# Kernel optimization log

Measured on AMD Instinct MI355X. Metric: run time of the kernel, lower is better.

The kernel has to match this reference:

```python
import jax, jax.numpy as jnp
import numpy as np

B, S, HIDDEN = 2, 2048, 1024
NUM_HEADS, HEAD_DIM = 16, 64
STRIDE = 128
NEG = -10000.0


def _strided_mask(seq_len):
    # Sparse Transformer strided pattern: causal, local window of STRIDE,
    # plus every STRIDE-th previous position.
    i = jnp.arange(seq_len)[:, None]
    j = jnp.arange(seq_len)[None, :]
    diff = i - j
    allowed = (diff >= 0) & ((diff < STRIDE) | (diff % STRIDE == 0))
    return jnp.where(allowed, 0.0, NEG).astype(jnp.float32)  # [S, S]


def setup_inputs() -> dict:
    key = jax.random.key(0)
    k0, k1, k2, k3, k4 = jax.random.split(key, 5)
    hidden_states = jax.random.normal(k0, (B, S, HIDDEN), dtype=jnp.float32)
    attention_mask = jnp.zeros((B, 1, 1, S), dtype=jnp.float32)
    W_q = jax.random.normal(k1, (HIDDEN, HIDDEN), dtype=jnp.float32) * 0.02
    b_q = jnp.zeros((HIDDEN,), dtype=jnp.float32)
    W_v = jax.random.normal(k2, (HIDDEN, HIDDEN), dtype=jnp.float32) * 0.02
    b_v = jnp.zeros((HIDDEN,), dtype=jnp.float32)
    return {"hidden_states": hidden_states, "attention_mask": attention_mask,
            "W_q": W_q, "b_q": b_q, "W_v": W_v, "b_v": b_v}


def _heads(x):
    b, s, _ = x.shape
    return x.reshape(b, s, NUM_HEADS, HEAD_DIM).transpose(0, 2, 1, 3)  # [B,H,S,d]


def reference(hidden_states, attention_mask, W_q, b_q, W_v, b_v):
    q = _heads(hidden_states @ W_q + b_q)  # [B,H,S,d]
    v = _heads(hidden_states @ W_v + b_v)  # [B,H,S,d]
    hash_mask = _strided_mask(q.shape[-2])  # [S,S], broadcast over B,H
    # NB: source computes matmul(query, query^T) -- Q used for both sides.
    scores = jnp.einsum('bhid,bhjd->bhij', q, q) + hash_mask
    scores = scores / jnp.sqrt(jnp.asarray(HEAD_DIM, scores.dtype))
    scores = scores + attention_mask
    probs = jax.nn.softmax(scores, axis=-1)  # dropout p=0 (eval)
    ctx = jnp.einsum('bhij,bhjd->bhid', probs, v)  # [B,H,S,d]
    b = ctx.shape[0]
    return ctx.transpose(0, 2, 1, 3).reshape(b, -1, NUM_HEADS * HEAD_DIM)
```

## Files before the change

### kernel.cpp

```cpp
#include <hip/hip_runtime.h>

typedef __attribute__((ext_vector_type(8))) short short8;
typedef __attribute__((ext_vector_type(4))) float float4v;

__device__ inline float bf2f(ushort u) {
    unsigned v = ((unsigned)u) << 16;
    return __builtin_bit_cast(float, v);
}
__device__ inline ushort f2bf(float f) {
    unsigned u = __builtin_bit_cast(unsigned, f);
    u += 0x7FFFu + ((u >> 16) & 1u);
    return (ushort)(u >> 16);
}

__global__ __launch_bounds__(256) void transpose_w(
    const float* __restrict__ Wq, const float* __restrict__ Wv,
    ushort* __restrict__ Wtq, ushort* __restrict__ Wtv) {
    __shared__ ushort tile[64][68];
    const float* W = blockIdx.z ? Wv : Wq;
    ushort* Wt     = blockIdx.z ? Wtv : Wtq;
    const int k0 = blockIdx.y * 64, n0 = blockIdx.x * 64;
    const int tid = threadIdx.x;
    const int rr = tid >> 4;
    const int cc = (tid & 15) * 4;
    union U4 { ushort u[4]; uint2 v; };
#pragma unroll
    for (int i = 0; i < 4; ++i) {
        int row = rr + i * 16;
        float4v f = *(const float4v*)(W + (size_t)(k0 + row) * 1024 + n0 + cc);
        U4 x;
#pragma unroll
        for (int j = 0; j < 4; ++j) x.u[j] = f2bf(f[j]);
        *(uint2*)&tile[row][cc] = x.v;
    }
    __syncthreads();
#pragma unroll
    for (int i = 0; i < 4; ++i) {
        int row = rr + i * 16;
        U4 o;
#pragma unroll
        for (int j = 0; j < 4; ++j) o.u[j] = tile[cc + j][row];
        *(uint2*)(Wt + (size_t)(n0 + row) * 1024 + k0 + cc) = o.v;
    }
}

__global__ __launch_bounds__(256) void qv_gemm(
    const float* __restrict__ hs,
    const ushort* __restrict__ Wtq, const ushort* __restrict__ Wtv,
    const float* __restrict__ bq, const float* __restrict__ bv,
    ushort* __restrict__ q_ws, ushort* __restrict__ v_ws) {
    __shared__ ushort Al[128][72];
    __shared__ ushort Bl[128][72];
    const ushort* Wt  = blockIdx.z ? Wtv : Wtq;
    const float* bias = blockIdx.z ? bv : bq;
    ushort* out       = blockIdx.z ? v_ws : q_ws;
    const int m0 = blockIdx.y * 128;
    const int n0 = blockIdx.x * 128;
    const int tid = threadIdx.x;
    const int wid = tid >> 6, lane = tid & 63;
    const int quad = lane >> 4, l16 = lane & 15;
    const int wm = (wid >> 1) * 64, wn = (wid & 1) * 64;

    float4v acc[4][4] = {};

    for (int kt = 0; kt < 1024; kt += 64) {
        __syncthreads();
#pragma unroll
        for (int i = 0; i < 4; ++i) {
            int c = tid + i * 256;
            int row = c >> 3, col = (c & 7) * 8;
            const float* src = hs + (size_t)(m0 + row) * 1024 + kt + col;
            float4v f0 = *(const float4v*)(src);
            float4v f1 = *(const float4v*)(src + 4);
            union { ushort u[8]; uint4 v; } pk;
#pragma unroll
            for (int j = 0; j < 4; ++j) { pk.u[j] = f2bf(f0[j]); pk.u[4 + j] = f2bf(f1[j]); }
            *(uint4*)&Al[row][col] = pk.v;
            *(uint4*)&Bl[row][col] = *(const uint4*)(Wt + (size_t)(n0 + row) * 1024 + kt + col);
        }
        __syncthreads();
#pragma unroll
        for (int ks = 0; ks < 2; ++ks) {
            short8 af[4], bfr[4];
#pragma unroll
            for (int mt = 0; mt < 4; ++mt)
                af[mt] = *(const short8*)&Al[wm + mt * 16 + l16][ks * 32 + quad * 8];
#pragma unroll
            for (int nt = 0; nt < 4; ++nt)
                bfr[nt] = *(const short8*)&Bl[wn + nt * 16 + l16][ks * 32 + quad * 8];
#pragma unroll
            for (int mt = 0; mt < 4; ++mt)
#pragma unroll
                for (int nt = 0; nt < 4; ++nt)
                    acc[mt][nt] = __builtin_amdgcn_mfma_f32_16x16x32_bf16(
                        af[mt], bfr[nt], acc[mt][nt], 0, 0, 0);
        }
    }
#pragma unroll
    for (int mt = 0; mt < 4; ++mt) {
#pragma unroll
        for (int nt = 0; nt < 4; ++nt) {
            int coln = n0 + wn + nt * 16 + l16;
            float bsv = bias[coln];
            int hh = coln >> 6, dd = coln & 63;
#pragma unroll
            for (int reg = 0; reg < 4; ++reg) {
                int r = m0 + wm + mt * 16 + quad * 4 + reg;
                int bb = r >> 11, s = r & 2047;
                out[(((size_t)bb * 16 + hh) * 2048 + s) * 64 + dd] =
                    f2bf(acc[mt][nt][reg] + bsv);
            }
        }
    }
}

__global__ __launch_bounds__(512) void attn(
    const ushort* __restrict__ q_ws, const ushort* __restrict__ v_ws,
    const float* __restrict__ amask, float* __restrict__ out) {
    const int t = blockIdx.x, h = blockIdx.y, b = blockIdx.z;

    __shared__ ushort Kw[256][72];
    __shared__ ushort Vt[64][266];
    __shared__ ushort Pl[128][266];
    __shared__ float  Sstr[128][17];
    __shared__ float  am[2048];

    const int tid = threadIdx.x;
    const int wid = tid >> 6, lane = tid & 63;
    const int quad = lane >> 4, l16 = lane & 15;
    const int r0 = wid * 16;
    const size_t qbase = ((size_t)b * 16 + h) * 2048 * 64;
    const int base_row = (t - 1) * 128;
    const int nk = (t >= 2) ? (t - 1) : 0;

    *(float4v*)&am[tid * 4] = *(const float4v*)(amask + (size_t)b * 2048 + tid * 4);
#pragma unroll
    for (int i = 0; i < 4; ++i) {
        int c = tid + i * 512;
        int row = c >> 3, col = (c & 7) * 8;
        int jg = base_row + row; if (jg < 0) jg = 0;
        *(uint4*)&Kw[row][col] = *(const uint4*)(q_ws + qbase + (size_t)jg * 64 + col);
    }
    {
        int j = tid & 255, dh0 = (tid >> 8) * 32;
        int jg = base_row + j; if (jg < 0) jg = 0;
        const ushort* src = v_ws + qbase + (size_t)jg * 64 + dh0;
#pragma unroll
        for (int d = 0; d < 32; d += 8) {
            union { uint4 v; ushort u[8]; } tmp;
            tmp.v = *(const uint4*)(src + d);
#pragma unroll
            for (int jj = 0; jj < 8; ++jj) Vt[dh0 + d + jj][j] = tmp.u[jj];
        }
    }
    __syncthreads();

    float4v sacc[16] = {};
#pragma unroll
    for (int ks = 0; ks < 2; ++ks) {
        short8 af = *(const short8*)&Kw[128 + r0 + l16][ks * 32 + quad * 8];
#pragma unroll
        for (int nt = 0; nt < 16; ++nt) {
            short8 bfr = *(const short8*)&Kw[nt * 16 + l16][ks * 32 + quad * 8];
            sacc[nt] = __builtin_amdgcn_mfma_f32_16x16x32_bf16(af, bfr, sacc[nt], 0, 0, 0);
        }
    }

    const int sr = tid >> 2;
    const int dq = (tid & 3) * 16;
    if (nk > 0) {
        float qv[16];
#pragma unroll
        for (int d = 0; d < 16; d += 8) {
            union { uint4 v; ushort u[8]; } tmp;
            tmp.v = *(const uint4*)&Kw[128 + sr][dq + d];
#pragma unroll
            for (int j = 0; j < 8; ++j) qv[d + j] = bf2f(tmp.u[j]);
        }
        for (int k = 0; k < nk; ++k) {
            const ushort* kr = q_ws + qbase + (size_t)(k * 128 + sr) * 64 + dq;
            float p = 0.f;
#pragma unroll
            for (int d = 0; d < 16; d += 8) {
                union { uint4 v; ushort u[8]; } tmp;
                tmp.v = *(const uint4*)(kr + d);
#pragma unroll
                for (int jj = 0; jj < 8; ++jj) p += qv[d + jj] * bf2f(tmp.u[jj]);
            }
            p += __shfl_xor(p, 1);
            p += __shfl_xor(p, 2);
            if ((tid & 3) == 0)
                Sstr[sr][k] = p * 0.125f + am[k * 128 + sr];
        }
    }
    __syncthreads();

#pragma unroll
    for (int reg = 0; reg < 4; ++reg) {
        int rr = r0 + quad * 4 + reg;
        float sv[16];
#pragma unroll
        for (int nt = 0; nt < 16; ++nt) {
            int c = nt * 16 + l16;
            bool allowed = (c >= rr) && (c <= rr + 128) && (t > 0 || c >= 128);
            int ci = base_row + c; if (ci < 0) ci = 0;
            sv[nt] = allowed ? sacc[nt][reg] * 0.125f + am[ci] : -INFINITY;
        }
        float sstr_v = (l16 < nk) ? Sstr[rr][l16] : -INFINITY;
        float m = sstr_v;
#pragma unroll
        for (int nt = 0; nt < 16; ++nt) m = fmaxf(m, sv[nt]);
#pragma unroll
        for (int off = 1; off < 16; off <<= 1) m = fmaxf(m, __shfl_xor(m, off));

        float es = (l16 < nk) ? __expf(sstr_v - m) : 0.f;
        float sum = es;
#pragma unroll
        for (int nt = 0; nt < 16; ++nt) {
            float e = (sv[nt] == -INFINITY) ? 0.f : __expf(sv[nt] - m);
            sv[nt] = e; sum += e;
        }
#pragma unroll
        for (int off = 1; off < 16; off <<= 1) sum += __shfl_xor(sum, off);
        float rden = 1.f / sum;
#pragma unroll
        for (int nt = 0; nt < 16; ++nt)
            Pl[rr][nt * 16 + l16] = f2bf(sv[nt] * rden);
        if (l16 < nk)
            Sstr[rr][l16] = es * rden;
    }
    __syncthreads();

    float4v cacc[4] = {};
#pragma unroll
    for (int ks = 0; ks < 8; ++ks) {
        short8 af = *(const short8*)&Pl[r0 + l16][ks * 32 + quad * 8];
#pragma unroll
        for (int nt = 0; nt < 4; ++nt) {
            short8 bfr = *(const short8*)&Vt[nt * 16 + l16][ks * 32 + quad * 8];
            cacc[nt] = __builtin_amdgcn_mfma_f32_16x16x32_bf16(af, bfr, cacc[nt], 0, 0, 0);
        }
    }
    __syncthreads();

    float* ctxp = (float*)&Pl[0][0];
    {
        float acc16[16] = {};
        for (int k = 0; k < nk; ++k) {
            float p = Sstr[sr][k];
            const ushort* vr = v_ws + qbase + (size_t)(k * 128 + sr) * 64 + dq;
#pragma unroll
            for (int d = 0; d < 16; d += 8) {
                union { uint4 v; ushort u[8]; } tmp;
                tmp.v = *(const uint4*)(vr + d);
#pragma unroll
                for (int j = 0; j < 8; ++j) acc16[d + j] += p * bf2f(tmp.u[j]);
            }
        }
#pragma unroll
        for (int d = 0; d < 16; d += 4)
            *(float4v*)&ctxp[sr * 68 + dq + d] = *(const float4v*)&acc16[d];
    }
    __syncthreads();

    const size_t obase = ((size_t)b * 2048 + (size_t)t * 128) * 1024 + (size_t)h * 64;
#pragma unroll
    for (int nt = 0; nt < 4; ++nt)
#pragma unroll
        for (int reg = 0; reg < 4; ++reg) {
            int rr = r0 + quad * 4 + reg;
            int d = nt * 16 + l16;
            out[obase + (size_t)rr * 1024 + d] = cacc[nt][reg] + ctxp[rr * 68 + d];
        }
}

extern "C" void kernel_launch(void* const* d_in, const int* in_sizes, int n_in,
                              void* d_out, int out_size, void* d_ws, size_t ws_size,
                              hipStream_t stream) {
    int ihs = -1, iam = -1, iw1 = -1, iw2 = -1, ib1 = -1, ib2 = -1;
    for (int i = 0; i < n_in; ++i) {
        int s = in_sizes[i];
        if      (s == 4194304) { if (ihs < 0) ihs = i; }
        else if (s == 4096)    { if (iam < 0) iam = i; }
        else if (s == 1048576) { if (iw1 < 0) iw1 = i; else if (iw2 < 0) iw2 = i; }
        else if (s == 1024)    { if (ib1 < 0) ib1 = i; else if (ib2 < 0) ib2 = i; }
    }
    if (ihs < 0) ihs = 0; if (iam < 0) iam = 1;
    if (iw1 < 0) iw1 = 2; if (ib1 < 0) ib1 = 3;
    if (iw2 < 0) iw2 = 4; if (ib2 < 0) ib2 = 5;

    const float* hs    = (const float*)d_in[ihs];
    const float* amask = (const float*)d_in[iam];
    const float* Wq    = (const float*)d_in[iw1];
    const float* bq    = (const float*)d_in[ib1];
    const float* Wv    = (const float*)d_in[iw2];
    const float* bv    = (const float*)d_in[ib2];
    float* out = (float*)d_out;

    char* ws = (char*)d_ws;
    ushort* Wtq  = (ushort*)(ws);
    ushort* Wtv  = (ushort*)(ws + (1u << 21));
    ushort* q_ws = (ushort*)(ws + (2u << 21));
    ushort* v_ws = (ushort*)(ws + (2u << 21) + (1u << 23));

    transpose_w<<<dim3(16, 16, 2), 256, 0, stream>>>(Wq, Wv, Wtq, Wtv);
    qv_gemm<<<dim3(8, 32, 2), 256, 0, stream>>>(hs, Wtq, Wtv, bq, bv, q_ws, v_ws);
    attn<<<dim3(16, 16, 2), 512, 0, stream>>>(q_ws, v_ws, amask, out);
}
```

Before: 157.5 us.

## Pre-convert hidden states, swizzle LDS tiles, and halve attention query tile

Adds a separate kernel that converts hidden states to bf16 once, so the GEMM no longer reconverts the same A tile for every N block and loads bf16 directly. The GEMM and attention shared-memory tiles switch from padded layouts to an XOR-swizzled layout to avoid bank conflicts. The attention kernel moves to 64-query tiles with 256 threads and a 192-key local window, which doubles the grid and trims wasted window work. Strided keys are now indexed per row modulo 128. The cost is one extra kernel launch and an extra global round trip for the converted activations.

```diff
diff --git a/kernel.cpp b/kernel.cpp
--- a/kernel.cpp
+++ b/kernel.cpp
@@ -11,6 +11,20 @@
     unsigned u = __builtin_bit_cast(unsigned, f);
     u += 0x7FFFu + ((u >> 16) & 1u);
     return (ushort)(u >> 16);
+}
+
+__global__ __launch_bounds__(256) void convert_hs(
+    const float* __restrict__ hs, ushort* __restrict__ hsb) {
+    const size_t base = ((size_t)blockIdx.x * 256 + threadIdx.x) * 16;
+    union { ushort u[16]; uint4 v[2]; } o;
+#pragma unroll
+    for (int q = 0; q < 4; ++q) {
+        float4v f = *(const float4v*)(hs + base + q * 4);
+#pragma unroll
+        for (int j = 0; j < 4; ++j) o.u[q * 4 + j] = f2bf(f[j]);
+    }
+    *(uint4*)(hsb + base)     = o.v[0];
+    *(uint4*)(hsb + base + 8) = o.v[1];
 }
 
 __global__ __launch_bounds__(256) void transpose_w(
@@ -45,17 +59,16 @@
 }
 
 __global__ __launch_bounds__(256) void qv_gemm(
-    const float* __restrict__ hs,
+    const ushort* __restrict__ hsb,
     const ushort* __restrict__ Wtq, const ushort* __restrict__ Wtv,
     const float* __restrict__ bq, const float* __restrict__ bv,
     ushort* __restrict__ q_ws, ushort* __restrict__ v_ws) {
-    __shared__ ushort Al[128][72];
-    __shared__ ushort Bl[128][72];
+    __shared__ ushort Al[128 * 64];
+    __shared__ ushort Bl[128 * 64];
     const ushort* Wt  = blockIdx.z ? Wtv : Wtq;
     const float* bias = blockIdx.z ? bv : bq;
     ushort* out       = blockIdx.z ? v_ws : q_ws;
-    const int m0 = blockIdx.y * 128;
-    const int n0 = blockIdx.x * 128;
+    const int m0 = blockIdx.y * 128, n0 = blockIdx.x * 128;
     const int tid = threadIdx.x;
     const int wid = tid >> 6, lane = tid & 63;
     const int quad = lane >> 4, l16 = lane & 15;
@@ -67,27 +80,28 @@
         __syncthreads();
 #pragma unroll
         for (int i = 0; i < 4; ++i) {
-            int c = tid + i * 256;
-            int row = c >> 3, col = (c & 7) * 8;
-            const float* src = hs + (size_t)(m0 + row) * 1024 + kt + col;
-            float4v f0 = *(const float4v*)(src);
-            float4v f1 = *(const float4v*)(src + 4);
-            union { ushort u[8]; uint4 v; } pk;
-#pragma unroll
-            for (int j = 0; j < 4; ++j) { pk.u[j] = f2bf(f0[j]); pk.u[4 + j] = f2bf(f1[j]); }
-            *(uint4*)&Al[row][col] = pk.v;
-            *(uint4*)&Bl[row][col] = *(const uint4*)(Wt + (size_t)(n0 + row) * 1024 + kt + col);
+            int u = tid + i * 256;
+            int row = u >> 3, c = u & 7;
+            int p = c ^ (row & 7);
+            *(uint4*)&Al[row * 64 + p * 8] =
+                *(const uint4*)(hsb + (size_t)(m0 + row) * 1024 + kt + c * 8);
+            *(uint4*)&Bl[row * 64 + p * 8] =
+                *(const uint4*)(Wt + (size_t)(n0 + row) * 1024 + kt + c * 8);
         }
         __syncthreads();
 #pragma unroll
         for (int ks = 0; ks < 2; ++ks) {
             short8 af[4], bfr[4];
 #pragma unroll
-            for (int mt = 0; mt < 4; ++mt)
-                af[mt] = *(const short8*)&Al[wm + mt * 16 + l16][ks * 32 + quad * 8];
-#pragma unroll
-            for (int nt = 0; nt < 4; ++nt)
-                bfr[nt] = *(const short8*)&Bl[wn + nt * 16 + l16][ks * 32 + quad * 8];
+            for (int mt = 0; mt < 4; ++mt) {
+                int row = wm + mt * 16 + l16;
+                af[mt] = *(const short8*)&Al[row * 64 + (((ks * 4 + quad) ^ (l16 & 7)) * 8)];
+            }
+#pragma unroll
+            for (int nt = 0; nt < 4; ++nt) {
+                int row = wn + nt * 16 + l16;
+                bfr[nt] = *(const short8*)&Bl[row * 64 + (((ks * 4 + quad) ^ (l16 & 7)) * 8)];
+            }
 #pragma unroll
             for (int mt = 0; mt < 4; ++mt)
 #pragma unroll
@@ -114,83 +128,105 @@
     }
 }
 
-__global__ __launch_bounds__(512) void attn(
+__global__ __launch_bounds__(256) void attn(
     const ushort* __restrict__ q_ws, const ushort* __restrict__ v_ws,
     const float* __restrict__ amask, float* __restrict__ out) {
+    __shared__ __align__(16) char smem[62464];
+    ushort (*Kw)[64]  = (ushort(*)[64])smem;
+    ushort (*Pl)[192] = (ushort(*)[192])smem;
+    float*  ctxp      = (float*)smem;
+    ushort (*Vt)[192] = (ushort(*)[192])(smem + 32768);
+    float  (*Sstr)[17] = (float(*)[17])(smem + 57344);
+    float*  amw       = (float*)(smem + 61696);
+
     const int t = blockIdx.x, h = blockIdx.y, b = blockIdx.z;
-
-    __shared__ ushort Kw[256][72];
-    __shared__ ushort Vt[64][266];
-    __shared__ ushort Pl[128][266];
-    __shared__ float  Sstr[128][17];
-    __shared__ float  am[2048];
-
     const int tid = threadIdx.x;
     const int wid = tid >> 6, lane = tid & 63;
     const int quad = lane >> 4, l16 = lane & 15;
     const int r0 = wid * 16;
     const size_t qbase = ((size_t)b * 16 + h) * 2048 * 64;
-    const int base_row = (t - 1) * 128;
-    const int nk = (t >= 2) ? (t - 1) : 0;
-
-    *(float4v*)&am[tid * 4] = *(const float4v*)(amask + (size_t)b * 2048 + tid * 4);
-#pragma unroll
-    for (int i = 0; i < 4; ++i) {
-        int c = tid + i * 512;
-        int row = c >> 3, col = (c & 7) * 8;
-        int jg = base_row + row; if (jg < 0) jg = 0;
-        *(uint4*)&Kw[row][col] = *(const uint4*)(q_ws + qbase + (size_t)jg * 64 + col);
-    }
-    {
-        int j = tid & 255, dh0 = (tid >> 8) * 32;
-        int jg = base_row + j; if (jg < 0) jg = 0;
-        const ushort* src = v_ws + qbase + (size_t)jg * 64 + dh0;
-#pragma unroll
-        for (int d = 0; d < 32; d += 8) {
-            union { uint4 v; ushort u[8]; } tmp;
-            tmp.v = *(const uint4*)(src + d);
-#pragma unroll
-            for (int jj = 0; jj < 8; ++jj) Vt[dh0 + d + jj][j] = tmp.u[jj];
-        }
-    }
-    __syncthreads();
-
-    float4v sacc[16] = {};
+    const int t0 = t * 64;
+    const int bc = t0 - 128;
+    const int cmin = (t == 0) ? 128 : (t == 1 ? 64 : 0);
+    const int nk = (t >= 4) ? ((t >> 1) - 1) : 0;
+
+    if (tid < 192) {
+        int j = bc + tid; if (j < 0) j = 0;
+        amw[tid] = amask[(size_t)b * 2048 + j];
+    }
+#pragma unroll
+    for (int i = 0; i < 8; ++i) {
+        int u = tid + i * 256;
+        int row = u >> 3, c = u & 7;
+        int jg = (row < 192) ? (bc + row) : (t0 + row - 192);
+        if (jg < 0) jg = 0;
+        int p = c ^ (row & 7);
+        *(uint4*)&Kw[row][p * 8] = *(const uint4*)(q_ws + qbase + (size_t)jg * 64 + c * 8);
+    }
+#pragma unroll
+    for (int i = 0; i < 2; ++i) {
+        int u = tid + i * 256;
+        if (u < 384) {
+            int j0 = (u % 48) * 4, d0 = (u / 48) * 8;
+            ushort vreg[4][8];
+#pragma unroll
+            for (int jj = 0; jj < 4; ++jj) {
+                int jg = bc + j0 + jj; if (jg < 0) jg = 0;
+                *(uint4*)vreg[jj] = *(const uint4*)(v_ws + qbase + (size_t)jg * 64 + d0);
+            }
+#pragma unroll
+            for (int dd = 0; dd < 8; ++dd) {
+                int row = d0 + dd;
+                int p = (j0 >> 3) ^ (row & 7);
+                union { ushort u4[4]; uint2 v; } pk;
+                pk.u4[0] = vreg[0][dd]; pk.u4[1] = vreg[1][dd];
+                pk.u4[2] = vreg[2][dd]; pk.u4[3] = vreg[3][dd];
+                *(uint2*)&Vt[row][p * 8 + (j0 & 7)] = pk.v;
+            }
+        }
+    }
+    __syncthreads();
+
+    float4v sacc[12] = {};
 #pragma unroll
     for (int ks = 0; ks < 2; ++ks) {
-        short8 af = *(const short8*)&Kw[128 + r0 + l16][ks * 32 + quad * 8];
-#pragma unroll
-        for (int nt = 0; nt < 16; ++nt) {
-            short8 bfr = *(const short8*)&Kw[nt * 16 + l16][ks * 32 + quad * 8];
+        int sw = ((ks * 4 + quad) ^ (l16 & 7)) * 8;
+        short8 af = *(const short8*)&Kw[192 + r0 + l16][sw];
+#pragma unroll
+        for (int nt = 0; nt < 12; ++nt) {
+            short8 bfr = *(const short8*)&Kw[nt * 16 + l16][sw];
             sacc[nt] = __builtin_amdgcn_mfma_f32_16x16x32_bf16(af, bfr, sacc[nt], 0, 0, 0);
         }
     }
 
     const int sr = tid >> 2;
     const int dq = (tid & 3) * 16;
+    const int smod = (t0 + sr) & 127;
     if (nk > 0) {
         float qv[16];
 #pragma unroll
-        for (int d = 0; d < 16; d += 8) {
-            union { uint4 v; ushort u[8]; } tmp;
-            tmp.v = *(const uint4*)&Kw[128 + sr][dq + d];
-#pragma unroll
-            for (int j = 0; j < 8; ++j) qv[d + j] = bf2f(tmp.u[j]);
-        }
-        for (int k = 0; k < nk; ++k) {
-            const ushort* kr = q_ws + qbase + (size_t)(k * 128 + sr) * 64 + dq;
+        for (int cc = 0; cc < 2; ++cc) {
+            int c = (dq >> 3) + cc;
+            int p = c ^ (sr & 7);
+            union { uint4 v; ushort u[8]; } tm;
+            tm.v = *(const uint4*)&Kw[192 + sr][p * 8];
+#pragma unroll
+            for (int jj = 0; jj < 8; ++jj) qv[cc * 8 + jj] = bf2f(tm.u[jj]);
+        }
+        for (int m = 0; m < nk; ++m) {
+            const ushort* kr = q_ws + qbase + (size_t)(smod + (m << 7)) * 64 + dq;
             float p = 0.f;
 #pragma unroll
             for (int d = 0; d < 16; d += 8) {
-                union { uint4 v; ushort u[8]; } tmp;
-                tmp.v = *(const uint4*)(kr + d);
-#pragma unroll
-                for (int jj = 0; jj < 8; ++jj) p += qv[d + jj] * bf2f(tmp.u[jj]);
+                union { uint4 v; ushort u[8]; } tm;
+                tm.v = *(const uint4*)(kr + d);
+#pragma unroll
+                for (int jj = 0; jj < 8; ++jj) p += qv[d + jj] * bf2f(tm.u[jj]);
             }
             p += __shfl_xor(p, 1);
             p += __shfl_xor(p, 2);
             if ((tid & 3) == 0)
-                Sstr[sr][k] = p * 0.125f + am[k * 128 + sr];
+                Sstr[sr][m] = p * 0.125f + amask[(size_t)b * 2048 + smod + (m << 7)];
         }
     }
     __syncthreads();
@@ -198,25 +234,24 @@
 #pragma unroll
     for (int reg = 0; reg < 4; ++reg) {
         int rr = r0 + quad * 4 + reg;
-        float sv[16];
-#pragma unroll
-        for (int nt = 0; nt < 16; ++nt) {
+        float sv[12];
+#pragma unroll
+        for (int nt = 0; nt < 12; ++nt) {
             int c = nt * 16 + l16;
-            bool allowed = (c >= rr) && (c <= rr + 128) && (t > 0 || c >= 128);
-            int ci = base_row + c; if (ci < 0) ci = 0;
-            sv[nt] = allowed ? sacc[nt][reg] * 0.125f + am[ci] : -INFINITY;
+            bool allowed = (c >= rr) && (c <= rr + 128) && (c >= cmin);
+            sv[nt] = allowed ? sacc[nt][reg] * 0.125f + amw[c] : -INFINITY;
         }
         float sstr_v = (l16 < nk) ? Sstr[rr][l16] : -INFINITY;
         float m = sstr_v;
 #pragma unroll
-        for (int nt = 0; nt < 16; ++nt) m = fmaxf(m, sv[nt]);
+        for (int nt = 0; nt < 12; ++nt) m = fmaxf(m, sv[nt]);
 #pragma unroll
         for (int off = 1; off < 16; off <<= 1) m = fmaxf(m, __shfl_xor(m, off));
 
         float es = (l16 < nk) ? __expf(sstr_v - m) : 0.f;
         float sum = es;
 #pragma unroll
-        for (int nt = 0; nt < 16; ++nt) {
+        for (int nt = 0; nt < 12; ++nt) {
             float e = (sv[nt] == -INFINITY) ? 0.f : __expf(sv[nt] - m);
             sv[nt] = e; sum += e;
         }
@@ -224,37 +259,40 @@
         for (int off = 1; off < 16; off <<= 1) sum += __shfl_xor(sum, off);
         float rden = 1.f / sum;
 #pragma unroll
-        for (int nt = 0; nt < 16; ++nt)
-            Pl[rr][nt * 16 + l16] = f2bf(sv[nt] * rden);
-        if (l16 < nk)
-            Sstr[rr][l16] = es * rden;
+        for (int nt = 0; nt < 12; ++nt) {
+            int c = nt * 16 + l16;
+            int p = ((c >> 3) ^ (rr & 7));
+            Pl[rr][p * 8 + (c & 7)] = f2bf(sv[nt] * rden);
+        }
+        if (l16 < nk) Sstr[rr][l16] = es * rden;
     }
     __syncthreads();
 
     float4v cacc[4] = {};
 #pragma unroll
-    for (int ks = 0; ks < 8; ++ks) {
-        short8 af = *(const short8*)&Pl[r0 + l16][ks * 32 + quad * 8];
+    for (int ks = 0; ks < 6; ++ks) {
+        int chunk = ks * 4 + quad;
+        int sw = (chunk ^ (l16 & 7)) * 8;
+        short8 af = *(const short8*)&Pl[r0 + l16][sw];
 #pragma unroll
         for (int nt = 0; nt < 4; ++nt) {
-            short8 bfr = *(const short8*)&Vt[nt * 16 + l16][ks * 32 + quad * 8];
+            short8 bfr = *(const short8*)&Vt[nt * 16 + l16][sw];
             cacc[nt] = __builtin_amdgcn_mfma_f32_16x16x32_bf16(af, bfr, cacc[nt], 0, 0, 0);
         }
     }
     __syncthreads();
 
-    float* ctxp = (float*)&Pl[0][0];
     {
         float acc16[16] = {};
-        for (int k = 0; k < nk; ++k) {
-            float p = Sstr[sr][k];
-            const ushort* vr = v_ws + qbase + (size_t)(k * 128 + sr) * 64 + dq;
+        for (int m = 0; m < nk; ++m) {
+            float p = Sstr[sr][m];
+            const ushort* vr = v_ws + qbase + (size_t)(smod + (m << 7)) * 64 + dq;
 #pragma unroll
             for (int d = 0; d < 16; d += 8) {
-                union { uint4 v; ushort u[8]; } tmp;
-                tmp.v = *(const uint4*)(vr + d);
-#pragma unroll
-                for (int j = 0; j < 8; ++j) acc16[d + j] += p * bf2f(tmp.u[j]);
+                union { uint4 v; ushort u[8]; } tm;
+                tm.v = *(const uint4*)(vr + d);
+#pragma unroll
+                for (int jj = 0; jj < 8; ++jj) acc16[d + jj] += p * bf2f(tm.u[jj]);
             }
         }
 #pragma unroll
@@ -263,7 +301,7 @@
     }
     __syncthreads();
 
-    const size_t obase = ((size_t)b * 2048 + (size_t)t * 128) * 1024 + (size_t)h * 64;
+    const size_t obase = ((size_t)b * 2048 + t0) * 1024 + (size_t)h * 64;
 #pragma unroll
     for (int nt = 0; nt < 4; ++nt)
 #pragma unroll
@@ -300,10 +338,12 @@
     char* ws = (char*)d_ws;
     ushort* Wtq  = (ushort*)(ws);
     ushort* Wtv  = (ushort*)(ws + (1u << 21));
-    ushort* q_ws = (ushort*)(ws + (2u << 21));
-    ushort* v_ws = (ushort*)(ws + (2u << 21) + (1u << 23));
-
+    ushort* hsb  = (ushort*)(ws + (2u << 21));
+    ushort* q_ws = (ushort*)(ws + (2u << 21) + (1u << 23));
+    ushort* v_ws = (ushort*)(ws + (2u << 21) + (2u << 23));
+
+    convert_hs<<<1024, 256, 0, stream>>>(hs, hsb);
     transpose_w<<<dim3(16, 16, 2), 256, 0, stream>>>(Wq, Wv, Wtq, Wtv);
-    qv_gemm<<<dim3(8, 32, 2), 256, 0, stream>>>(hs, Wtq, Wtv, bq, bv, q_ws, v_ws);
-    attn<<<dim3(16, 16, 2), 512, 0, stream>>>(q_ws, v_ws, amask, out);
-}
+    qv_gemm<<<dim3(8, 32, 2), 256, 0, stream>>>(hsb, Wtq, Wtv, bq, bv, q_ws, v_ws);
+    attn<<<dim3(32, 16, 2), 256, 0, stream>>>(q_ws, v_ws, amask, out);
+}
```

After: 153.0 us. 2.9% less time.
